# Kernel optimization log

Measured on AMD Instinct MI355X. Metric: run time of the kernel, lower is better.

Reference implementation:

```python
import jax, jax.numpy as jnp
import numpy as np

N = 100_000        # nodes
E = 3_200_000      # edges (avg degree 32)
F_IN = 2000        # highly-variable genes
H = 16             # hidden dim
C = 3              # KMeans clusters / classes


def setup_inputs() -> dict:
    key = jax.random.key(0)
    k1, k2, k3, k4 = jax.random.split(key, 4)
    x = jax.random.normal(k1, (N, F_IN), dtype=jnp.float32)
    edge_index = jax.random.randint(k2, (2, E), 0, N, dtype=jnp.int32)
    W1 = jax.random.normal(k3, (F_IN, H), dtype=jnp.float32) * (1.0 / np.sqrt(F_IN))
    b1 = jnp.zeros((H,), dtype=jnp.float32)
    W2 = jax.random.normal(k4, (H, C), dtype=jnp.float32) * (1.0 / np.sqrt(H))
    b2 = jnp.zeros((C,), dtype=jnp.float32)
    return {"x": x, "edge_index": edge_index, "W1": W1, "b1": b1, "W2": W2, "b2": b2}


def _gcn_conv(x, W, b, src, dst, n):
    """PyG GCNConv: linear -> add self-loops -> sym-normalized scatter-add -> +bias."""
    h = x @ W                                   # [N, F_out]
    loop = jnp.arange(n, dtype=src.dtype)
    src_sl = jnp.concatenate([src, loop])       # [E+N]
    dst_sl = jnp.concatenate([dst, loop])
    deg = jax.ops.segment_sum(jnp.ones(src_sl.shape[0], dtype=h.dtype), dst_sl, num_segments=n)
    dinv = jax.lax.rsqrt(deg)                   # deg >= 1 due to self-loops
    norm = dinv[src_sl] * dinv[dst_sl]          # [E+N]
    msg = h[src_sl] * norm[:, None]             # gather + scale
    out = jax.ops.segment_sum(msg, dst_sl, num_segments=n)  # scatter-add
    return out + b


def reference(x, edge_index, W1, b1, W2, b2):
    src, dst = edge_index[0], edge_index[1]
    n = x.shape[0]
    h = jax.nn.relu(_gcn_conv(x, W1, b1, src, dst, n))
    # F.dropout with training=False is identity (eval mode)
    logits = _gcn_conv(h, W2, b2, src, dst, n)
    return jax.nn.log_softmax(logits, axis=1)
```

## Files before the change

### kernel.cpp

```cpp
#include <hip/hip_runtime.h>
#include <hip/hip_bf16.h>


#define FIN   2000
#define HDIM  16
#define KB    40
#define NCHUNK (FIN / KB)
#define KSTRIDE 65

__global__ void zero_k(int4* __restrict__ p, int n4) {
    int i = blockIdx.x * 256 + threadIdx.x;
    if (i < n4) p[i] = make_int4(0, 0, 0, 0);
}

__global__ void count_k(const int* __restrict__ dst, int* __restrict__ cnt, int e) {
    int i = blockIdx.x * 256 + threadIdx.x;
    if (i < e) atomicAdd(&cnt[dst[i]], 1);
}

__global__ void dinv_k(const int* __restrict__ cnt, float* __restrict__ dinv, int n) {
    int i = blockIdx.x * 256 + threadIdx.x;
    if (i < n) dinv[i] = 1.0f / sqrtf((float)(cnt[i] + 1));
}

__global__ __launch_bounds__(1024) void scan_k(const int* __restrict__ cnt,
                                               int* __restrict__ rowptr, int n) {
    __shared__ int sdata[1024];
    int tid = threadIdx.x;
    int chunk = (n + 1023) >> 10;
    int s0 = tid * chunk;
    int s1 = s0 + chunk; if (s1 > n) s1 = n;
    int sum = 0;
    for (int i = s0; i < s1; ++i) sum += cnt[i];
    sdata[tid] = sum;
    __syncthreads();
    for (int off = 1; off < 1024; off <<= 1) {
        int v = sdata[tid];
        int u = (tid >= off) ? sdata[tid - off] : 0;
        __syncthreads();
        sdata[tid] = v + u;
        __syncthreads();
    }
    int run = sdata[tid] - sum;
    for (int i = s0; i < s1; ++i) { rowptr[i] = run; run += cnt[i]; }
    if (tid == 0) rowptr[n] = sdata[1023];
}

__global__ void scatter_k(const int* __restrict__ src, const int* __restrict__ dst,
                          const int* __restrict__ rowptr, int* __restrict__ cursor,
                          int* __restrict__ col, int e) {
    int i = blockIdx.x * 256 + threadIdx.x;
    if (i < e) {
        int d = dst[i];
        int pos = rowptr[d] + atomicAdd(&cursor[d], 1);
        col[pos] = src[i];
    }
}

__global__ __launch_bounds__(64) void gemm1(const float* __restrict__ x,
                                            const float* __restrict__ W1,
                                            const float* __restrict__ dinv,
                                            float* __restrict__ t1s, int n) {
    __shared__ float xT[2][KB * KSTRIDE];
    const int lane = threadIdx.x;
    const long base = (long)blockIdx.x * 64;

    float4 st[10];

#define STAGE_LOAD(c)                                                       \
    {                                                                       \
        _Pragma("unroll")                                                   \
        for (int i = 0; i < 10; ++i) {                                      \
            int job = i * 64 + lane;                                        \
            int jr = job / 10, jk = job - jr * 10;                          \
            long gr = base + jr; if (gr >= n) gr = n - 1;                   \
            st[i] = *(const float4*)(x + gr * FIN + (c) * KB + jk * 4);     \
        }                                                                   \
    }
#define STAGE_WRITE(bsel)                                                   \
    {                                                                       \
        float* p = &xT[(bsel)][0];                                          \
        _Pragma("unroll")                                                   \
        for (int i = 0; i < 10; ++i) {                                      \
            int job = i * 64 + lane;                                        \
            int jr = job / 10, jk = job - jr * 10;                          \
            p[(jk * 4 + 0) * KSTRIDE + jr] = st[i].x;                       \
            p[(jk * 4 + 1) * KSTRIDE + jr] = st[i].y;                       \
            p[(jk * 4 + 2) * KSTRIDE + jr] = st[i].z;                       \
            p[(jk * 4 + 3) * KSTRIDE + jr] = st[i].w;                       \
        }                                                                   \
    }

    float acc[HDIM];
#pragma unroll
    for (int j = 0; j < HDIM; ++j) acc[j] = 0.0f;

    STAGE_LOAD(0);
    STAGE_WRITE(0);

    for (int c = 0; c < NCHUNK; ++c) {
        int b = c & 1;
        if (c + 1 < NCHUNK) STAGE_LOAD(c + 1);
        const float* w0 = W1 + c * KB * HDIM;
#pragma unroll 4
        for (int k = 0; k < KB; ++k) {
            float xv = xT[b][k * KSTRIDE + lane];
            const float* w = w0 + k * HDIM;
#pragma unroll
            for (int j = 0; j < HDIM; ++j) acc[j] = fmaf(xv, w[j], acc[j]);
        }
        if (c + 1 < NCHUNK) STAGE_WRITE((c + 1) & 1);
    }

    long row = base + lane;
    long rc = row < n ? row : n - 1;
    float s = dinv[rc];
    if (row < n) {
        float4* o = (float4*)(t1s + row * HDIM);
        o[0] = make_float4(acc[0] * s, acc[1] * s, acc[2] * s, acc[3] * s);
        o[1] = make_float4(acc[4] * s, acc[5] * s, acc[6] * s, acc[7] * s);
        o[2] = make_float4(acc[8] * s, acc[9] * s, acc[10] * s, acc[11] * s);
        o[3] = make_float4(acc[12] * s, acc[13] * s, acc[14] * s, acc[15] * s);
    }
#undef STAGE_LOAD
#undef STAGE_WRITE
}

__global__ __launch_bounds__(256) void agg1(const float* __restrict__ t1s,
                                            const int* __restrict__ rowptr,
                                            const int* __restrict__ col,
                                            const float* __restrict__ dinv,
                                            const float* __restrict__ b1,
                                            const float* __restrict__ W2,
                                            float* __restrict__ t2s, int n) {
    int tid = blockIdx.x * 256 + threadIdx.x;
    int node = tid >> 4;
    int j = tid & 15;
    if (node >= n) return;
    float acc = t1s[node * HDIM + j];
    int e0 = rowptr[node], e1 = rowptr[node + 1];
    for (int e = e0; e < e1; ++e) {
        int s = col[e];
        acc += t1s[s * HDIM + j];
    }
    float dn = dinv[node];
    float h = acc * dn + b1[j];
    h = h > 0.0f ? h : 0.0f;
    float p0 = h * W2[j * 3 + 0];
    float p1 = h * W2[j * 3 + 1];
    float p2 = h * W2[j * 3 + 2];
#pragma unroll
    for (int off = 8; off > 0; off >>= 1) {
        p0 += __shfl_xor(p0, off, 16);
        p1 += __shfl_xor(p1, off, 16);
        p2 += __shfl_xor(p2, off, 16);
    }
    if (j == 0) {
        *(float4*)(t2s + node * 4) = make_float4(p0 * dn, p1 * dn, p2 * dn, 0.0f);
    }
}

__global__ __launch_bounds__(256) void agg2(const float* __restrict__ t2s,
                                            const int* __restrict__ rowptr,
                                            const int* __restrict__ col,
                                            const float* __restrict__ dinv,
                                            const float* __restrict__ b2,
                                            float* __restrict__ out, int n) {
    int node = blockIdx.x * 256 + threadIdx.x;
    if (node >= n) return;
    float4 a = *(const float4*)(t2s + node * 4);
    float a0 = a.x, a1 = a.y, a2 = a.z;
    int e0 = rowptr[node], e1 = rowptr[node + 1];
    for (int e = e0; e < e1; ++e) {
        int s = col[e];
        float4 v = *(const float4*)(t2s + s * 4);
        a0 += v.x; a1 += v.y; a2 += v.z;
    }
    float dn = dinv[node];
    float l0 = a0 * dn + b2[0];
    float l1 = a1 * dn + b2[1];
    float l2 = a2 * dn + b2[2];
    float m = fmaxf(l0, fmaxf(l1, l2));
    float lse = logf(expf(l0 - m) + expf(l1 - m) + expf(l2 - m)) + m;
    out[node * 3 + 0] = l0 - lse;
    out[node * 3 + 1] = l1 - lse;
    out[node * 3 + 2] = l2 - lse;
}

extern "C" void kernel_launch(void* const* d_in, const int* in_sizes, int n_in,
                              void* d_out, int out_size, void* d_ws, size_t ws_size,
                              hipStream_t stream) {
    const float* x  = (const float*)d_in[0];
    const int*   ei = (const int*)d_in[1];
    const float* W1 = (const float*)d_in[2];
    const float* b1 = (const float*)d_in[3];
    const float* W2 = (const float*)d_in[4];
    const float* b2 = (const float*)d_in[5];
    const int N = in_sizes[0] / FIN;
    const int E = in_sizes[1] / 2;
    const int* src = ei;
    const int* dst = ei + E;

    char* ws = (char*)d_ws;
    auto alloc = [&](size_t bytes) {
        char* p = ws;
        ws += (bytes + 255) & ~(size_t)255;
        return p;
    };
    size_t npad = ((size_t)N * 4 + 255) & ~(size_t)255;
    int*   cnt    = (int*)alloc(N * 4);
    int*   cursor = (int*)alloc(N * 4);
    int*   rowptr = (int*)alloc((size_t)(N + 1) * 4);
    float* dinv   = (float*)alloc(N * 4);
    int*   col    = (int*)alloc((size_t)E * 4);
    float* t1s    = (float*)alloc((size_t)N * HDIM * 4);
    float* t2s    = (float*)alloc((size_t)N * 4 * 4);

    int n4 = (int)(npad * 2 / 16);
    zero_k<<<(n4 + 255) / 256, 256, 0, stream>>>((int4*)cnt, n4);
    count_k<<<(E + 255) / 256, 256, 0, stream>>>(dst, cnt, E);
    dinv_k<<<(N + 255) / 256, 256, 0, stream>>>(cnt, dinv, N);
    scan_k<<<1, 1024, 0, stream>>>(cnt, rowptr, N);
    scatter_k<<<(E + 255) / 256, 256, 0, stream>>>(src, dst, rowptr, cursor, col, E);
    gemm1<<<(N + 63) / 64, 64, 0, stream>>>(x, W1, dinv, t1s, N);
    agg1<<<(N * 16 + 255) / 256, 256, 0, stream>>>(t1s, rowptr, col, dinv, b1, W2, t2s, N);
    agg2<<<(N + 255) / 256, 256, 0, stream>>>(t2s, rowptr, col, dinv, b2, (float*)d_out, N);
}
```

Measured before the change: 827.4 us.

## Vectorize CSR build, fold dinv into scan, split agg1 edges across 4 sub-groups

The count and scatter kernels now handle four edges per thread using int4 loads of src/dst. The dinv computation is folded into the single-block scan kernel, which removes one launch. agg1 now gives each node a full 64-lane wavefront: four groups of 16 lanes stride through its edges and combine their partial sums with shuffles. This raises memory-level parallelism for the gather-heavy aggregation, and agg2's loop gets an unroll hint. In exchange, the single-block scan does extra serial dinv work and summation order changes slightly.

```diff
diff --git a/kernel.cpp b/kernel.cpp
--- a/kernel.cpp
+++ b/kernel.cpp
@@ -14,24 +14,32 @@
 }
 
 __global__ void count_k(const int* __restrict__ dst, int* __restrict__ cnt, int e) {
-    int i = blockIdx.x * 256 + threadIdx.x;
-    if (i < e) atomicAdd(&cnt[dst[i]], 1);
-}
-
-__global__ void dinv_k(const int* __restrict__ cnt, float* __restrict__ dinv, int n) {
-    int i = blockIdx.x * 256 + threadIdx.x;
-    if (i < n) dinv[i] = 1.0f / sqrtf((float)(cnt[i] + 1));
+    int i = (blockIdx.x * 256 + threadIdx.x) * 4;
+    if (i + 3 < e) {
+        int4 d = *(const int4*)(dst + i);
+        atomicAdd(&cnt[d.x], 1);
+        atomicAdd(&cnt[d.y], 1);
+        atomicAdd(&cnt[d.z], 1);
+        atomicAdd(&cnt[d.w], 1);
+    } else {
+        for (int k = i; k < e; ++k) atomicAdd(&cnt[dst[k]], 1);
+    }
 }
 
 __global__ __launch_bounds__(1024) void scan_k(const int* __restrict__ cnt,
-                                               int* __restrict__ rowptr, int n) {
+                                               int* __restrict__ rowptr,
+                                               float* __restrict__ dinv, int n) {
     __shared__ int sdata[1024];
     int tid = threadIdx.x;
     int chunk = (n + 1023) >> 10;
     int s0 = tid * chunk;
     int s1 = s0 + chunk; if (s1 > n) s1 = n;
     int sum = 0;
-    for (int i = s0; i < s1; ++i) sum += cnt[i];
+    for (int i = s0; i < s1; ++i) {
+        int c = cnt[i];
+        dinv[i] = 1.0f / sqrtf((float)(c + 1));
+        sum += c;
+    }
     sdata[tid] = sum;
     __syncthreads();
     for (int off = 1; off < 1024; off <<= 1) {
@@ -49,11 +57,19 @@
 __global__ void scatter_k(const int* __restrict__ src, const int* __restrict__ dst,
                           const int* __restrict__ rowptr, int* __restrict__ cursor,
                           int* __restrict__ col, int e) {
-    int i = blockIdx.x * 256 + threadIdx.x;
-    if (i < e) {
-        int d = dst[i];
-        int pos = rowptr[d] + atomicAdd(&cursor[d], 1);
-        col[pos] = src[i];
+    int i = (blockIdx.x * 256 + threadIdx.x) * 4;
+    if (i + 3 < e) {
+        int4 d = *(const int4*)(dst + i);
+        int4 s = *(const int4*)(src + i);
+        col[rowptr[d.x] + atomicAdd(&cursor[d.x], 1)] = s.x;
+        col[rowptr[d.y] + atomicAdd(&cursor[d.y], 1)] = s.y;
+        col[rowptr[d.z] + atomicAdd(&cursor[d.z], 1)] = s.z;
+        col[rowptr[d.w] + atomicAdd(&cursor[d.w], 1)] = s.w;
+    } else {
+        for (int k = i; k < e; ++k) {
+            int d = dst[k];
+            col[rowptr[d] + atomicAdd(&cursor[d], 1)] = src[k];
+        }
     }
 }
 
@@ -133,16 +149,18 @@
                                             const float* __restrict__ b1,
                                             const float* __restrict__ W2,
                                             float* __restrict__ t2s, int n) {
-    int tid = blockIdx.x * 256 + threadIdx.x;
-    int node = tid >> 4;
-    int j = tid & 15;
+    int node = blockIdx.x * 4 + (threadIdx.x >> 6);
     if (node >= n) return;
-    float acc = t1s[node * HDIM + j];
+    int lane = threadIdx.x & 63;
+    int nb = lane >> 4;
+    int j  = lane & 15;
     int e0 = rowptr[node], e1 = rowptr[node + 1];
-    for (int e = e0; e < e1; ++e) {
-        int s = col[e];
-        acc += t1s[s * HDIM + j];
-    }
+    float acc = (nb == 0) ? t1s[node * HDIM + j] : 0.0f;
+    for (int e = e0 + nb; e < e1; e += 4) {
+        acc += t1s[col[e] * HDIM + j];
+    }
+    acc += __shfl_xor(acc, 16);
+    acc += __shfl_xor(acc, 32);
     float dn = dinv[node];
     float h = acc * dn + b1[j];
     h = h > 0.0f ? h : 0.0f;
@@ -155,7 +173,7 @@
         p1 += __shfl_xor(p1, off, 16);
         p2 += __shfl_xor(p2, off, 16);
     }
-    if (j == 0) {
+    if (lane == 0) {
         *(float4*)(t2s + node * 4) = make_float4(p0 * dn, p1 * dn, p2 * dn, 0.0f);
     }
 }
@@ -171,6 +189,7 @@
     float4 a = *(const float4*)(t2s + node * 4);
     float a0 = a.x, a1 = a.y, a2 = a.z;
     int e0 = rowptr[node], e1 = rowptr[node + 1];
+#pragma unroll 4
     for (int e = e0; e < e1; ++e) {
         int s = col[e];
         float4 v = *(const float4*)(t2s + s * 4);
@@ -218,11 +237,11 @@
 
     int n4 = (int)(npad * 2 / 16);
     zero_k<<<(n4 + 255) / 256, 256, 0, stream>>>((int4*)cnt, n4);
-    count_k<<<(E + 255) / 256, 256, 0, stream>>>(dst, cnt, E);
-    dinv_k<<<(N + 255) / 256, 256, 0, stream>>>(cnt, dinv, N);
-    scan_k<<<1, 1024, 0, stream>>>(cnt, rowptr, N);
-    scatter_k<<<(E + 255) / 256, 256, 0, stream>>>(src, dst, rowptr, cursor, col, E);
+    int e4 = (E + 3) / 4;
+    count_k<<<(e4 + 255) / 256, 256, 0, stream>>>(dst, cnt, E);
+    scan_k<<<1, 1024, 0, stream>>>(cnt, rowptr, dinv, N);
+    scatter_k<<<(e4 + 255) / 256, 256, 0, stream>>>(src, dst, rowptr, cursor, col, E);
     gemm1<<<(N + 63) / 64, 64, 0, stream>>>(x, W1, dinv, t1s, N);
-    agg1<<<(N * 16 + 255) / 256, 256, 0, stream>>>(t1s, rowptr, col, dinv, b1, W2, t2s, N);
+    agg1<<<(N + 3) / 4, 256, 0, stream>>>(t1s, rowptr, col, dinv, b1, W2, t2s, N);
     agg2<<<(N + 255) / 256, 256, 0, stream>>>(t2s, rowptr, col, dinv, b2, (float*)d_out, N);
 }
```

New measurement: 857.7 us. +3.7%, slower.
